# Kernel optimization log

Measured on AMD Instinct MI355X. Metric: run time of the kernel, lower is better.

## Reference

```python
import jax, jax.numpy as jnp
import numpy as np

SCALE = 0.02

def setup_inputs() -> dict:
    key = jax.random.key(0)
    k1, k2 = jax.random.split(key)
    B, D, T, H = 2, 1024, 2048, 16
    x = jax.random.normal(k1, (B, D, T), dtype=jnp.float32)
    qkv = jax.random.normal(k2, (3, H, D, D // H), dtype=jnp.float32) * SCALE
    return {"x": x, "qkv": qkv}

def reference(x, qkv):
    B, D, T = x.shape
    H = qkv.shape[1]
    # fused QKV projection: (B,D,T) x (3,H,D,Dh) -> (3,B,H,T,Dh)
    proj = jnp.einsum('bdt,nhdD->nbhtD', x, qkv)
    q, k, v = proj[0], proj[1], proj[2]
    scale = jnp.sqrt(jnp.asarray(D // H, dtype=x.dtype))
    # scores: (B,H,T,T)
    attn = jax.nn.softmax(jnp.einsum('bhtD,bhTD->bhtT', q, k) / scale, axis=-1)
    # weighted values, head dim placed before time: (B,H,Dh,T)
    out = jnp.einsum('bhtT,bhTD->bhDt', attn, v)
    return out.reshape(B, D, T)
```

## Files before the change

kernel.cpp:

```cpp
#include <hip/hip_runtime.h>

#define B_ 2
#define D_ 1024
#define T_ 2048
#define H_ 16
#define DH_ 64
#define BH_ (B_ * H_)

typedef __attribute__((ext_vector_type(8))) short bf16x8;
typedef __attribute__((ext_vector_type(8))) unsigned short u16x8;
typedef __attribute__((ext_vector_type(4))) float f32x4;

__device__ __forceinline__ unsigned cvt_pk_bf16(float a, float b) {
    unsigned r;
    asm("v_cvt_pk_bf16_f32 %0, %1, %2" : "=v"(r) : "v"(a), "v"(b));
    return r;
}

__global__ __launch_bounds__(256) void xpose_kernel(
    const float* __restrict__ x, unsigned short* __restrict__ xT)
{
    __shared__ __align__(16) unsigned short Ls[64][68];
    const int t0 = blockIdx.x * 64;
    const int d0 = blockIdx.y * 64;
    const int b  = blockIdx.z;
    const int tid = threadIdx.x;

    const float* xb = x + (size_t)b * D_ * T_ + (size_t)d0 * T_ + t0;
    #pragma unroll
    for (int p = 0; p < 4; p++) {
        int i4  = tid + p * 256;
        int row = i4 >> 4;
        int c4  = (i4 & 15) << 2;
        float4 v = *(const float4*)(xb + (size_t)row * T_ + c4);
        uint2 u;
        u.x = cvt_pk_bf16(v.x, v.y);
        u.y = cvt_pk_bf16(v.z, v.w);
        *(uint2*)&Ls[row][c4] = u;
    }
    __syncthreads();
    unsigned short* ob = xT + (size_t)b * T_ * D_ + (size_t)t0 * D_ + d0;
    #pragma unroll
    for (int p = 0; p < 2; p++) {
        int i    = tid + p * 256;
        int orow = i >> 3;
        int oc8  = (i & 7) * 8;
        u16x8 tv;
        #pragma unroll
        for (int j = 0; j < 8; j++) tv[j] = Ls[oc8 + j][orow];
        *(u16x8*)(ob + (size_t)orow * D_ + oc8) = tv;
    }
}

__global__ __launch_bounds__(256) void wpose_kernel(
    const float* __restrict__ w, unsigned short* __restrict__ wT)
{
    __shared__ __align__(16) unsigned short Ls[64][68];
    const int d0 = blockIdx.x * 64;
    const int nh = blockIdx.y;
    const int tid = threadIdx.x;

    const float* wb = w + (size_t)nh * D_ * DH_ + (size_t)d0 * DH_;
    #pragma unroll
    for (int p = 0; p < 4; p++) {
        int i4  = tid + p * 256;
        int row = i4 >> 4;
        int c4  = (i4 & 15) << 2;
        float4 v = *(const float4*)(wb + (size_t)row * DH_ + c4);
        uint2 u;
        u.x = cvt_pk_bf16(v.x, v.y);
        u.y = cvt_pk_bf16(v.z, v.w);
        *(uint2*)&Ls[row][c4] = u;
    }
    __syncthreads();
    unsigned short* ob = wT + (size_t)nh * DH_ * D_ + d0;
    #pragma unroll
    for (int p = 0; p < 2; p++) {
        int i    = tid + p * 256;
        int orow = i >> 3;
        int oc8  = (i & 7) * 8;
        u16x8 tv;
        #pragma unroll
        for (int j = 0; j < 8; j++) tv[j] = Ls[oc8 + j][orow];
        *(u16x8*)(ob + (size_t)orow * D_ + oc8) = tv;
    }
}

#define LX 80

__global__ __launch_bounds__(256, 3) void proj_mfma_kernel(
    const unsigned short* __restrict__ xT, const unsigned short* __restrict__ wT,
    unsigned short* __restrict__ qk, unsigned short* __restrict__ vT)
{
    __shared__ __align__(16) unsigned short Buf[20480];
    unsigned short* Xs = Buf;
    unsigned short* Ws = Buf + 10240;
    unsigned short* Es = Buf;

    const int t0 = blockIdx.x * 128;
    const int y  = blockIdx.y;
    const int n  = y >> 4;
    const int b  = (y >> 3) & 1;
    const int hp = y & 7;

    const unsigned short* xb = xT + (size_t)b * T_ * D_ + (size_t)t0 * D_;
    const unsigned short* wb = wT + (size_t)(n * 16 + 2 * hp) * DH_ * D_;

    const int tid  = threadIdx.x;
    const int wv   = tid >> 6;
    const int lane = tid & 63;
    const int c15  = lane & 15;
    const int quad = lane >> 4;
    const int tq   = (wv & 1) * 64;
    const int dq   = (wv >> 1) * 64;

    const int srow = tid >> 3;
    const int scol = (tid & 7) * 8;

    f32x4 acc[4][4];
    #pragma unroll
    for (int mt = 0; mt < 4; mt++)
        #pragma unroll
        for (int nt = 0; nt < 4; nt++)
            acc[mt][nt] = (f32x4){0.f, 0.f, 0.f, 0.f};

    u16x8 xreg[4], wreg[4];
    #pragma unroll
    for (int p = 0; p < 4; p++) {
        int row = srow + p * 32;
        xreg[p] = *(const u16x8*)(xb + (size_t)row * D_ + scol);
        wreg[p] = *(const u16x8*)(wb + (size_t)row * D_ + scol);
    }

    for (int k0 = 0; k0 < D_; k0 += 64) {
        __syncthreads();
        #pragma unroll
        for (int p = 0; p < 4; p++) {
            int row = srow + p * 32;
            *(u16x8*)&Xs[row * LX + scol] = xreg[p];
            *(u16x8*)&Ws[row * LX + scol] = wreg[p];
        }
        __syncthreads();

        if (k0 + 64 < D_) {
            #pragma unroll
            for (int p = 0; p < 4; p++) {
                int row = srow + p * 32;
                xreg[p] = *(const u16x8*)(xb + (size_t)row * D_ + k0 + 64 + scol);
                wreg[p] = *(const u16x8*)(wb + (size_t)row * D_ + k0 + 64 + scol);
            }
        }

        bf16x8 af[4][2], bf[4][2];
        #pragma unroll
        for (int mt = 0; mt < 4; mt++)
            #pragma unroll
            for (int s = 0; s < 2; s++)
                af[mt][s] = *(bf16x8*)&Xs[(tq + mt * 16 + c15) * LX + quad * 8 + s * 32];
        #pragma unroll
        for (int nt = 0; nt < 4; nt++)
            #pragma unroll
            for (int s = 0; s < 2; s++)
                bf[nt][s] = *(bf16x8*)&Ws[(dq + nt * 16 + c15) * LX + quad * 8 + s * 32];

        #pragma unroll
        for (int mt = 0; mt < 4; mt++)
            #pragma unroll
            for (int nt = 0; nt < 4; nt++)
                #pragma unroll
                for (int s = 0; s < 2; s++)
                    acc[mt][nt] = __builtin_amdgcn_mfma_f32_16x16x32_bf16(
                        af[mt][s], bf[nt][s], acc[mt][nt], 0, 0, 0);
    }

    const float scale = (n == 0) ? 0.125f * 1.44269504f : 1.0f;
    __syncthreads();
    #pragma unroll
    for (int mt = 0; mt < 4; mt++)
        #pragma unroll
        for (int nt = 0; nt < 4; nt++)
            #pragma unroll
            for (int r = 0; r < 4; r++) {
                float v = acc[mt][nt][r] * scale;
                Es[(tq + mt * 16 + quad * 4 + r) * 136 + dq + nt * 16 + c15] =
                    (unsigned short)cvt_pk_bf16(v, v);
            }
    __syncthreads();

    if (n < 2) {
        #pragma unroll
        for (int p = 0; p < 8; p++) {
            int i    = tid + p * 256;
            int row  = i >> 4;
            int col8 = (i & 15) * 8;
            int head = col8 >> 6;
            unsigned short* ob = qk +
                ((size_t)(n * 32 + b * 16 + 2 * hp + head) * T_ + t0 + row) * DH_ + (col8 & 63);
            *(u16x8*)ob = *(u16x8*)&Es[row * 136 + col8];
        }
    } else {
        #pragma unroll
        for (int p = 0; p < 8; p++) {
            int i    = tid + p * 256;
            int orow = i >> 4;
            int oc8  = (i & 15) * 8;
            int head = orow >> 6;
            u16x8 tv;
            #pragma unroll
            for (int j = 0; j < 8; j++) tv[j] = Es[(oc8 + j) * 136 + orow];
            unsigned short* ob = vT +
                (size_t)(b * 16 + 2 * hp + head) * DH_ * T_ +
                (size_t)(orow & 63) * T_ + t0 + oc8;
            *(u16x8*)ob = tv;
        }
    }
}

__global__ __launch_bounds__(256, 4) void attn_mfma_kernel(
    const unsigned short* __restrict__ qk, const unsigned short* __restrict__ vT,
    float* __restrict__ out)
{
    __shared__ __align__(16) unsigned short Sm[20480];

    const int flat = blockIdx.x;
    const int bh   = (flat & 7) * 4 + ((flat >> 3) >> 5);
    const int t0   = ((flat >> 3) & 31) * 64;

    const unsigned short* qg = qk + ((size_t)bh * T_ + t0) * DH_;
    const unsigned short* kg = qk + ((size_t)(BH_ + bh) * T_) * DH_;
    const unsigned short* vg = vT + (size_t)bh * DH_ * T_;

    const int tid  = threadIdx.x;
    const int wv   = tid >> 6;
    const int lane = tid & 63;
    const int c15  = lane & 15;
    const int quad = lane >> 4;
    const int swz  = (c15 & 7) * 8;
    const int h7   = c15 & 7;

    unsigned short* Ps = Sm + 16384 + wv * 1024;

    const int srow = tid >> 3;
    const int sch  = tid & 7;
    const int ssw  = ((sch ^ (srow & 7)) * 8);

    bf16x8 bq[2];
    #pragma unroll
    for (int s = 0; s < 2; s++)
        bq[s] = *(const bf16x8*)(qg + (size_t)(wv * 16 + c15) * DH_ + quad * 8 + s * 32);

    float lsum = 0.f;
    f32x4 Oacc[4];
    #pragma unroll
    for (int nt = 0; nt < 4; nt++) Oacc[nt] = (f32x4){0.f, 0.f, 0.f, 0.f};

    u16x8 kreg[2], vreg[2];
    #pragma unroll
    for (int p = 0; p < 2; p++) {
        int row = srow + p * 32;
        kreg[p] = *(const u16x8*)(kg + (size_t)row * DH_ + sch * 8);
        vreg[p] = *(const u16x8*)(vg + (size_t)row * T_ + sch * 8);
    }
    #pragma unroll
    for (int p = 0; p < 2; p++) {
        int row = srow + p * 32;
        *(u16x8*)&Sm[row * 64 + ssw]        = kreg[p];
        *(u16x8*)&Sm[4096 + row * 64 + ssw] = vreg[p];
    }

    for (int tau = 0; tau < T_; tau += 64) {
        const int cur = (tau >> 6) & 1;
        unsigned short* Ks = Sm + cur * 8192;
        unsigned short* Vs = Ks + 4096;
        __syncthreads();

        const bool pf = (tau + 64 < T_);
        if (pf) {
            #pragma unroll
            for (int p = 0; p < 2; p++) {
                int row = srow + p * 32;
                kreg[p] = *(const u16x8*)(kg + (size_t)(tau + 64 + row) * DH_ + sch * 8);
                vreg[p] = *(const u16x8*)(vg + (size_t)row * T_ + tau + 64 + sch * 8);
            }
        }

        #pragma unroll
        for (int mt = 0; mt < 4; mt++) {
            f32x4 sa = (f32x4){0.f, 0.f, 0.f, 0.f};
            #pragma unroll
            for (int s = 0; s < 2; s++) {
                bf16x8 ak = *(bf16x8*)&Ks[(mt * 16 + c15) * 64 +
                                          (((quad + 4 * s) ^ h7) * 8)];
                sa = __builtin_amdgcn_mfma_f32_16x16x32_bf16(ak, bq[s], sa, 0, 0, 0);
            }
            float p0 = __builtin_amdgcn_exp2f(sa[0]);
            float p1 = __builtin_amdgcn_exp2f(sa[1]);
            float p2 = __builtin_amdgcn_exp2f(sa[2]);
            float p3 = __builtin_amdgcn_exp2f(sa[3]);
            lsum += (p0 + p1) + (p2 + p3);
            uint2 pk;
            pk.x = cvt_pk_bf16(p0, p1);
            pk.y = cvt_pk_bf16(p2, p3);
            *(uint2*)&Ps[c15 * 64 + ((mt * 16 + quad * 4) ^ swz)] = pk;
        }

        #pragma unroll
        for (int s = 0; s < 2; s++) {
            bf16x8 ap = *(bf16x8*)&Ps[c15 * 64 + ((quad * 8 + s * 32) ^ swz)];
            #pragma unroll
            for (int nt = 0; nt < 4; nt++) {
                bf16x8 bv = *(bf16x8*)&Vs[(nt * 16 + c15) * 64 +
                                          (((quad + 4 * s) ^ h7) * 8)];
                Oacc[nt] = __builtin_amdgcn_mfma_f32_16x16x32_bf16(ap, bv, Oacc[nt], 0, 0, 0);
            }
        }

        if (pf) {
            unsigned short* Kn = Sm + (1 - cur) * 8192;
            #pragma unroll
            for (int p = 0; p < 2; p++) {
                int row = srow + p * 32;
                *(u16x8*)&Kn[row * 64 + ssw]        = kreg[p];
                *(u16x8*)&Kn[4096 + row * 64 + ssw] = vreg[p];
            }
        }
    }

    lsum += __shfl_xor(lsum, 16);
    lsum += __shfl_xor(lsum, 32);
    float linv[4];
    #pragma unroll
    for (int r = 0; r < 4; r++)
        linv[r] = 1.0f / __shfl(lsum, quad * 4 + r);

    __syncthreads();
    float* Osw = (float*)(void*)Sm + wv * 1088;
    #pragma unroll
    for (int nt = 0; nt < 4; nt++)
        #pragma unroll
        for (int r = 0; r < 4; r++)
            Osw[(nt * 16 + c15) * 17 + quad * 4 + r] = Oacc[nt][r] * linv[r];

    const int b = bh >> 4, h = bh & 15;
    float* og = out + (size_t)b * D_ * T_ + (size_t)(h * DH_) * T_ + t0 + wv * 16;
    #pragma unroll
    for (int p = 0; p < 4; p++) {
        int idx = lane + p * 64;
        int dh  = idx >> 2;
        int qs  = (idx & 3) * 4;
        float4 v = *(float4*)&Osw[dh * 17 + qs];
        *(float4*)(og + (size_t)dh * T_ + qs) = v;
    }
}

extern "C" void kernel_launch(void* const* d_in, const int* in_sizes, int n_in,
                              void* d_out, int out_size, void* d_ws, size_t ws_size,
                              hipStream_t stream)
{
    const float* x = (const float*)d_in[0];
    const float* w = (const float*)d_in[1];
    float* out = (float*)d_out;

    unsigned short* qk = (unsigned short*)d_ws;
    unsigned short* vT = (unsigned short*)((char*)d_ws + (24u << 20));
    unsigned short* xT = (unsigned short*)((char*)d_ws + (32u << 20));
    unsigned short* wT = (unsigned short*)((char*)d_ws + (40u << 20));

    xpose_kernel<<<dim3(T_ / 64, D_ / 64, B_), 256, 0, stream>>>(x, xT);
    wpose_kernel<<<dim3(D_ / 64, 3 * H_), 256, 0, stream>>>(w, wT);
    proj_mfma_kernel<<<dim3(T_ / 128, 48), 256, 0, stream>>>(xT, wT, qk, vT);
    attn_mfma_kernel<<<1024, 256, 0, stream>>>(qk, vT, out);
}
```

Measured before the change: 170.0 us.

## Split key dimension across waves and read K/V directly from global

Each wave now owns all 64 query rows but only one quarter of the key tiles, interleaved across waves. K and V fragments are read straight from global memory into registers instead of being staged through double-buffered shared memory. Partial outputs and row sums are reduced across waves through shared memory at the end. This removes per-tile block barriers and shared-memory staging, at the cost of more accumulator registers (lower occupancy bound of 3), uncoalesced global fragment loads, and a final cross-wave reduction.

```diff
diff --git a/kernel.cpp b/kernel.cpp
--- a/kernel.cpp
+++ b/kernel.cpp
@@ -216,19 +216,19 @@
     }
 }
 
-__global__ __launch_bounds__(256, 4) void attn_mfma_kernel(
+__global__ __launch_bounds__(256, 3) void attn_mfma_kernel(
     const unsigned short* __restrict__ qk, const unsigned short* __restrict__ vT,
     float* __restrict__ out)
 {
-    __shared__ __align__(16) unsigned short Sm[20480];
+    __shared__ __align__(16) unsigned short Sm[16640];
 
     const int flat = blockIdx.x;
     const int bh   = (flat & 7) * 4 + ((flat >> 3) >> 5);
     const int t0   = ((flat >> 3) & 31) * 64;
 
-    const unsigned short* qg = qk + ((size_t)bh * T_ + t0) * DH_;
-    const unsigned short* kg = qk + ((size_t)(BH_ + bh) * T_) * DH_;
-    const unsigned short* vg = vT + (size_t)bh * DH_ * T_;
+    const unsigned short* qgl = qk + ((size_t)bh * T_ + t0) * DH_;
+    const unsigned short* kg  = qk + ((size_t)(BH_ + bh) * T_) * DH_;
+    const unsigned short* vg  = vT + (size_t)bh * DH_ * T_;
 
     const int tid  = threadIdx.x;
     const int wv   = tid >> 6;
@@ -236,120 +236,115 @@
     const int c15  = lane & 15;
     const int quad = lane >> 4;
     const int swz  = (c15 & 7) * 8;
-    const int h7   = c15 & 7;
-
-    unsigned short* Ps = Sm + 16384 + wv * 1024;
-
-    const int srow = tid >> 3;
-    const int sch  = tid & 7;
-    const int ssw  = ((sch ^ (srow & 7)) * 8);
-
-    bf16x8 bq[2];
-    #pragma unroll
-    for (int s = 0; s < 2; s++)
-        bq[s] = *(const bf16x8*)(qg + (size_t)(wv * 16 + c15) * DH_ + quad * 8 + s * 32);
-
-    float lsum = 0.f;
-    f32x4 Oacc[4];
-    #pragma unroll
-    for (int nt = 0; nt < 4; nt++) Oacc[nt] = (f32x4){0.f, 0.f, 0.f, 0.f};
-
-    u16x8 kreg[2], vreg[2];
-    #pragma unroll
-    for (int p = 0; p < 2; p++) {
-        int row = srow + p * 32;
-        kreg[p] = *(const u16x8*)(kg + (size_t)row * DH_ + sch * 8);
-        vreg[p] = *(const u16x8*)(vg + (size_t)row * T_ + sch * 8);
-    }
-    #pragma unroll
-    for (int p = 0; p < 2; p++) {
-        int row = srow + p * 32;
-        *(u16x8*)&Sm[row * 64 + ssw]        = kreg[p];
-        *(u16x8*)&Sm[4096 + row * 64 + ssw] = vreg[p];
-    }
-
-    for (int tau = 0; tau < T_; tau += 64) {
-        const int cur = (tau >> 6) & 1;
-        unsigned short* Ks = Sm + cur * 8192;
-        unsigned short* Vs = Ks + 4096;
+
+    unsigned short* Ps = Sm + wv * 4096;
+
+    bf16x8 bq[4][2];
+    #pragma unroll
+    for (int g = 0; g < 4; g++)
+        #pragma unroll
+        for (int s = 0; s < 2; s++)
+            bq[g][s] = *(const bf16x8*)(qgl + (size_t)(g * 16 + c15) * DH_ + quad * 8 + s * 32);
+
+    float lsum[4] = {0.f, 0.f, 0.f, 0.f};
+    f32x4 Oacc[4][4];
+    #pragma unroll
+    for (int g = 0; g < 4; g++)
+        #pragma unroll
+        for (int nt = 0; nt < 4; nt++)
+            Oacc[g][nt] = (f32x4){0.f, 0.f, 0.f, 0.f};
+
+    for (int j = 0; j < 8; j++) {
+        const int tau = (wv + 4 * j) << 6;
+        const unsigned short* kt = kg + (size_t)tau * DH_;
+        const unsigned short* vt = vg + tau;
+
+        #pragma unroll
+        for (int mh = 0; mh < 2; mh++) {
+            bf16x8 akr[2][2];
+            #pragma unroll
+            for (int m2 = 0; m2 < 2; m2++)
+                #pragma unroll
+                for (int s = 0; s < 2; s++)
+                    akr[m2][s] = *(const bf16x8*)(
+                        kt + (size_t)((mh * 2 + m2) * 16 + c15) * DH_ + quad * 8 + s * 32);
+            #pragma unroll
+            for (int m2 = 0; m2 < 2; m2++) {
+                const int mt = mh * 2 + m2;
+                #pragma unroll
+                for (int g = 0; g < 4; g++) {
+                    f32x4 sa = (f32x4){0.f, 0.f, 0.f, 0.f};
+                    sa = __builtin_amdgcn_mfma_f32_16x16x32_bf16(akr[m2][0], bq[g][0], sa, 0, 0, 0);
+                    sa = __builtin_amdgcn_mfma_f32_16x16x32_bf16(akr[m2][1], bq[g][1], sa, 0, 0, 0);
+                    float p0 = __builtin_amdgcn_exp2f(sa[0]);
+                    float p1 = __builtin_amdgcn_exp2f(sa[1]);
+                    float p2 = __builtin_amdgcn_exp2f(sa[2]);
+                    float p3 = __builtin_amdgcn_exp2f(sa[3]);
+                    lsum[g] += (p0 + p1) + (p2 + p3);
+                    uint2 pk;
+                    pk.x = cvt_pk_bf16(p0, p1);
+                    pk.y = cvt_pk_bf16(p2, p3);
+                    *(uint2*)&Ps[g * 1024 + c15 * 64 + ((mt * 16 + quad * 4) ^ swz)] = pk;
+                }
+            }
+        }
+
+        #pragma unroll
+        for (int s = 0; s < 2; s++) {
+            bf16x8 bvr[4];
+            #pragma unroll
+            for (int nt = 0; nt < 4; nt++)
+                bvr[nt] = *(const bf16x8*)(vt + (size_t)(nt * 16 + c15) * T_ + s * 32 + quad * 8);
+            #pragma unroll
+            for (int g = 0; g < 4; g++) {
+                bf16x8 pa = *(bf16x8*)&Ps[g * 1024 + c15 * 64 + ((quad * 8 + s * 32) ^ swz)];
+                #pragma unroll
+                for (int nt = 0; nt < 4; nt++)
+                    Oacc[g][nt] = __builtin_amdgcn_mfma_f32_16x16x32_bf16(
+                        pa, bvr[nt], Oacc[g][nt], 0, 0, 0);
+            }
+        }
+    }
+
+    #pragma unroll
+    for (int g = 0; g < 4; g++) {
+        lsum[g] += __shfl_xor(lsum[g], 16);
+        lsum[g] += __shfl_xor(lsum[g], 32);
+    }
+
+    __syncthreads();
+    float* Obuf = (float*)(void*)Sm;
+    float* Lf   = (float*)(void*)Sm + 4352;
+    if (quad == 0) {
+        #pragma unroll
+        for (int g = 0; g < 4; g++)
+            Lf[wv * 64 + g * 16 + c15] = lsum[g];
+    }
+
+    const int b  = bh >> 4, h = bh & 15;
+    const int dh = tid >> 2;
+    const int qi = (tid & 3) * 4;
+    float* og = out + (size_t)b * D_ * T_ + (size_t)(h * DH_ + dh) * T_ + t0;
+
+    #pragma unroll
+    for (int g = 0; g < 4; g++) {
+        #pragma unroll
+        for (int nt = 0; nt < 4; nt++)
+            #pragma unroll
+            for (int r = 0; r < 4; r++)
+                Obuf[(wv * 16 + quad * 4 + r) * 68 + nt * 16 + c15] = Oacc[g][nt][r];
         __syncthreads();
-
-        const bool pf = (tau + 64 < T_);
-        if (pf) {
-            #pragma unroll
-            for (int p = 0; p < 2; p++) {
-                int row = srow + p * 32;
-                kreg[p] = *(const u16x8*)(kg + (size_t)(tau + 64 + row) * DH_ + sch * 8);
-                vreg[p] = *(const u16x8*)(vg + (size_t)row * T_ + tau + 64 + sch * 8);
-            }
-        }
-
-        #pragma unroll
-        for (int mt = 0; mt < 4; mt++) {
-            f32x4 sa = (f32x4){0.f, 0.f, 0.f, 0.f};
-            #pragma unroll
-            for (int s = 0; s < 2; s++) {
-                bf16x8 ak = *(bf16x8*)&Ks[(mt * 16 + c15) * 64 +
-                                          (((quad + 4 * s) ^ h7) * 8)];
-                sa = __builtin_amdgcn_mfma_f32_16x16x32_bf16(ak, bq[s], sa, 0, 0, 0);
-            }
-            float p0 = __builtin_amdgcn_exp2f(sa[0]);
-            float p1 = __builtin_amdgcn_exp2f(sa[1]);
-            float p2 = __builtin_amdgcn_exp2f(sa[2]);
-            float p3 = __builtin_amdgcn_exp2f(sa[3]);
-            lsum += (p0 + p1) + (p2 + p3);
-            uint2 pk;
-            pk.x = cvt_pk_bf16(p0, p1);
-            pk.y = cvt_pk_bf16(p2, p3);
-            *(uint2*)&Ps[c15 * 64 + ((mt * 16 + quad * 4) ^ swz)] = pk;
-        }
-
-        #pragma unroll
-        for (int s = 0; s < 2; s++) {
-            bf16x8 ap = *(bf16x8*)&Ps[c15 * 64 + ((quad * 8 + s * 32) ^ swz)];
-            #pragma unroll
-            for (int nt = 0; nt < 4; nt++) {
-                bf16x8 bv = *(bf16x8*)&Vs[(nt * 16 + c15) * 64 +
-                                          (((quad + 4 * s) ^ h7) * 8)];
-                Oacc[nt] = __builtin_amdgcn_mfma_f32_16x16x32_bf16(ap, bv, Oacc[nt], 0, 0, 0);
-            }
-        }
-
-        if (pf) {
-            unsigned short* Kn = Sm + (1 - cur) * 8192;
-            #pragma unroll
-            for (int p = 0; p < 2; p++) {
-                int row = srow + p * 32;
-                *(u16x8*)&Kn[row * 64 + ssw]        = kreg[p];
-                *(u16x8*)&Kn[4096 + row * 64 + ssw] = vreg[p];
-            }
-        }
-    }
-
-    lsum += __shfl_xor(lsum, 16);
-    lsum += __shfl_xor(lsum, 32);
-    float linv[4];
-    #pragma unroll
-    for (int r = 0; r < 4; r++)
-        linv[r] = 1.0f / __shfl(lsum, quad * 4 + r);
-
-    __syncthreads();
-    float* Osw = (float*)(void*)Sm + wv * 1088;
-    #pragma unroll
-    for (int nt = 0; nt < 4; nt++)
-        #pragma unroll
-        for (int r = 0; r < 4; r++)
-            Osw[(nt * 16 + c15) * 17 + quad * 4 + r] = Oacc[nt][r] * linv[r];
-
-    const int b = bh >> 4, h = bh & 15;
-    float* og = out + (size_t)b * D_ * T_ + (size_t)(h * DH_) * T_ + t0 + wv * 16;
-    #pragma unroll
-    for (int p = 0; p < 4; p++) {
-        int idx = lane + p * 64;
-        int dh  = idx >> 2;
-        int qs  = (idx & 3) * 4;
-        float4 v = *(float4*)&Osw[dh * 17 + qs];
-        *(float4*)(og + (size_t)dh * T_ + qs) = v;
+        float o[4];
+        #pragma unroll
+        for (int e = 0; e < 4; e++) {
+            int lq = g * 16 + qi + e;
+            float den = Lf[lq] + Lf[64 + lq] + Lf[128 + lq] + Lf[192 + lq];
+            float v = Obuf[(qi + e) * 68 + dh] + Obuf[(16 + qi + e) * 68 + dh]
+                    + Obuf[(32 + qi + e) * 68 + dh] + Obuf[(48 + qi + e) * 68 + dh];
+            o[e] = v / den;
+        }
+        *(float4*)(og + g * 16 + qi) = (float4){o[0], o[1], o[2], o[3]};
+        __syncthreads();
     }
 }
 
```

After: 211.3 us. 24.3% more time.

## Double-buffer projection GEMM tiles with direct global-to-LDS loads

Applied to the files above, without the earlier changes.

The QKV projection kernel now loads its X and W tiles with global_load_lds straight into shared memory, instead of staging them through registers. It uses two LDS buffers, so the next k-tile loads while the current one feeds the MFMAs. This drops the register staging, the LDS store instructions and one barrier per iteration. The cost is double the LDS footprint, a lower occupancy target (3 to 2 blocks per CU), and unpadded 64-element rows that may cause LDS bank conflicts on fragment reads.

```diff
diff --git a/kernel.cpp b/kernel.cpp
--- a/kernel.cpp
+++ b/kernel.cpp
@@ -15,6 +15,13 @@
     unsigned r;
     asm("v_cvt_pk_bf16_f32 %0, %1, %2" : "=v"(r) : "v"(a), "v"(b));
     return r;
+}
+
+__device__ __forceinline__ void gload_lds16(const unsigned short* g, unsigned short* l) {
+    __builtin_amdgcn_global_load_lds(
+        (const __attribute__((address_space(1))) unsigned int*)(const void*)g,
+        (__attribute__((address_space(3))) unsigned int*)(void*)l,
+        16, 0, 0);
 }
 
 __global__ __launch_bounds__(256) void xpose_kernel(
@@ -86,15 +93,11 @@
     }
 }
 
-#define LX 80
-
-__global__ __launch_bounds__(256, 3) void proj_mfma_kernel(
+__global__ __launch_bounds__(256, 2) void proj_mfma_kernel(
     const unsigned short* __restrict__ xT, const unsigned short* __restrict__ wT,
     unsigned short* __restrict__ qk, unsigned short* __restrict__ vT)
 {
-    __shared__ __align__(16) unsigned short Buf[20480];
-    unsigned short* Xs = Buf;
-    unsigned short* Ws = Buf + 10240;
+    __shared__ __align__(16) unsigned short Buf[32768];
     unsigned short* Es = Buf;
 
     const int t0 = blockIdx.x * 128;
@@ -114,8 +117,8 @@
     const int tq   = (wv & 1) * 64;
     const int dq   = (wv >> 1) * 64;
 
-    const int srow = tid >> 3;
-    const int scol = (tid & 7) * 8;
+    const int srow8 = lane >> 3;
+    const int sch8  = (lane & 7) * 8;
 
     f32x4 acc[4][4];
     #pragma unroll
@@ -124,44 +127,40 @@
         for (int nt = 0; nt < 4; nt++)
             acc[mt][nt] = (f32x4){0.f, 0.f, 0.f, 0.f};
 
-    u16x8 xreg[4], wreg[4];
-    #pragma unroll
-    for (int p = 0; p < 4; p++) {
-        int row = srow + p * 32;
-        xreg[p] = *(const u16x8*)(xb + (size_t)row * D_ + scol);
-        wreg[p] = *(const u16x8*)(wb + (size_t)row * D_ + scol);
-    }
-
-    for (int k0 = 0; k0 < D_; k0 += 64) {
+    auto stage = [&](int k0, int bsel) {
+        unsigned short* Xs = Buf + bsel * 16384;
+        unsigned short* Ws = Xs + 8192;
+        #pragma unroll
+        for (int i = 0; i < 4; i++) {
+            int row = wv * 32 + i * 8;
+            gload_lds16(xb + (size_t)(row + srow8) * D_ + k0 + sch8,
+                        Xs + row * 64);
+            gload_lds16(wb + (size_t)(row + srow8) * D_ + k0 + sch8,
+                        Ws + row * 64);
+        }
+    };
+
+    stage(0, 0);
+    int ks = 0;
+    for (int k0 = 0; k0 < D_; k0 += 64, ks ^= 1) {
         __syncthreads();
-        #pragma unroll
-        for (int p = 0; p < 4; p++) {
-            int row = srow + p * 32;
-            *(u16x8*)&Xs[row * LX + scol] = xreg[p];
-            *(u16x8*)&Ws[row * LX + scol] = wreg[p];
-        }
-        __syncthreads();
-
-        if (k0 + 64 < D_) {
-            #pragma unroll
-            for (int p = 0; p < 4; p++) {
-                int row = srow + p * 32;
-                xreg[p] = *(const u16x8*)(xb + (size_t)row * D_ + k0 + 64 + scol);
-                wreg[p] = *(const u16x8*)(wb + (size_t)row * D_ + k0 + 64 + scol);
-            }
-        }
+
+        if (k0 + 64 < D_) stage(k0 + 64, ks ^ 1);
+
+        unsigned short* Xs = Buf + ks * 16384;
+        unsigned short* Ws = Xs + 8192;
 
         bf16x8 af[4][2], bf[4][2];
         #pragma unroll
         for (int mt = 0; mt < 4; mt++)
             #pragma unroll
             for (int s = 0; s < 2; s++)
-                af[mt][s] = *(bf16x8*)&Xs[(tq + mt * 16 + c15) * LX + quad * 8 + s * 32];
+                af[mt][s] = *(bf16x8*)&Xs[(tq + mt * 16 + c15) * 64 + quad * 8 + s * 32];
         #pragma unroll
         for (int nt = 0; nt < 4; nt++)
             #pragma unroll
             for (int s = 0; s < 2; s++)
-                bf[nt][s] = *(bf16x8*)&Ws[(dq + nt * 16 + c15) * LX + quad * 8 + s * 32];
+                bf[nt][s] = *(bf16x8*)&Ws[(dq + nt * 16 + c15) * 64 + quad * 8 + s * 32];
 
         #pragma unroll
         for (int mt = 0; mt < 4; mt++)
```

Result: no change. 168.0 us (-1.2%).
